# Kernel optimization log

Measured on AMD Instinct MI355X. Metric: run time of the kernel, lower is better.

Reference implementation:

```python
import jax, jax.numpy as jnp
import numpy as np

B, T, NG, NP, DV = 256, 100, 4096, 512, 2


def setup_inputs() -> dict:
    key = jax.random.key(0)
    k = jax.random.split(key, 6)
    v = jax.random.normal(k[0], (B, T, DV), dtype=jnp.float32) * 0.1
    P0 = jax.random.uniform(k[1], (B, NP), dtype=jnp.float32)
    # Dense kernels (glorot-ish scale); recurrent kernel uniform(-0.02, 0.02) per the module
    W_enc = jax.random.normal(k[2], (NP, NG), dtype=jnp.float32) / np.sqrt(NP)
    W_in = jax.random.normal(k[3], (DV, NG), dtype=jnp.float32) / np.sqrt(DV)
    W_rec = (jax.random.uniform(k[4], (NG, NG), dtype=jnp.float32) * 2.0 - 1.0) * 0.02
    W_dec = jax.random.normal(k[5], (NG, NP), dtype=jnp.float32) / np.sqrt(NG)
    return {"v": v, "P0": P0, "W_enc": W_enc, "W_in": W_in, "W_rec": W_rec, "W_dec": W_dec}


def reference(v, P0, W_enc, W_in, W_rec, W_dec):
    # encoder: init hidden state from place-cell code P0  -> [B, Ng]
    h0 = P0 @ W_enc
    # Precompute input projection for all timesteps: [B, T, Ng] -> scan over T
    xW = jnp.einsum('btd,dg->btg', v, W_in)
    xW_t = jnp.swapaxes(xW, 0, 1)  # [T, B, Ng]

    def step(h, x):
        h_new = jax.nn.relu(x + h @ W_rec)
        return h_new, h_new

    _, g = jax.lax.scan(step, h0, xW_t)      # g: [T, B, Ng]
    g = jnp.swapaxes(g, 0, 1)                # [B, T, Ng]
    place_preds = jnp.einsum('btg,gp->btp', g, W_dec)  # [B, T, Np]
    return place_preds
```

## Files before the change

### kernel.cpp

```cpp
#include <hip/hip_runtime.h>
#include <hip/hip_bf16.h>

typedef __attribute__((ext_vector_type(8))) short bf16x8;
typedef __attribute__((ext_vector_type(4))) float f32x4;

#define MFMA __builtin_amdgcn_mfma_f32_16x16x32_bf16

__device__ __forceinline__ short f2bf(float f) {
    union { __hip_bfloat16 h; short s; } u;
    u.h = __float2bfloat16(f);
    return u.s;
}

__device__ __forceinline__ void gld_lds16(const void* g, void* l) {
    auto gp = (const __attribute__((address_space(1))) void*)(g);
    auto lp = (__attribute__((address_space(3))) void*)(l);
    __builtin_amdgcn_global_load_lds(gp, lp, 16, 0, 0);
}

__global__ __launch_bounds__(64) void cvt_tile(const float* __restrict__ in,
                                               __hip_bfloat16* __restrict__ out, int C) {
    const int cd32 = C >> 5;
    const int tile = blockIdx.x;
    const int r16 = tile / cd32, c32 = tile - r16 * cd32;
    const int l = threadIdx.x;
    const int row = (r16 << 4) + (l & 15);
    const int c0 = (c32 << 5) + ((l >> 4) << 3);
    const float* src = in + (size_t)row * C + c0;
    short o[8];
#pragma unroll
    for (int j = 0; j < 8; ++j) o[j] = f2bf(src[j]);
    *(bf16x8*)((char*)out + (size_t)tile * 1024 + (l << 4)) = *(bf16x8*)o;
}

__global__ __launch_bounds__(64) void tcvt_tile(const float* __restrict__ in,
                                                __hip_bfloat16* __restrict__ out,
                                                int N, int K) {
    const int kd32 = K >> 5;
    const int tile = blockIdx.x;
    const int n16 = tile / kd32, k32 = tile - n16 * kd32;
    const int l = threadIdx.x;
    const int n = (n16 << 4) + (l & 15);
    const int k0 = (k32 << 5) + ((l >> 4) << 3);
    short o[8];
#pragma unroll
    for (int j = 0; j < 8; ++j) o[j] = f2bf(in[(size_t)(k0 + j) * N + n]);
    *(bf16x8*)((char*)out + (size_t)tile * 1024 + (l << 4)) = *(bf16x8*)o;
}

template <int MODE, int NW, int KC>
__global__ __launch_bounds__(NW * 64) void gemm_w(const __hip_bfloat16* __restrict__ A,
                                                  const __hip_bfloat16* __restrict__ B,
                                                  void* __restrict__ outp,
                                                  const float* __restrict__ v,
                                                  const float* __restrict__ Wi, int t) {
    constexpr int KD32 = KC * NW;
    __shared__ __align__(16) char lds[NW * 16384];
    const int id = blockIdx.x;
    int bm, bn;
    if constexpr (MODE == 2) {
        int xcd = id & 7, idx = id >> 3;
        int sw = xcd * 400 + idx;
        bm = sw >> 3;
        bn = sw & 7;
    } else {
        int xcd = id & 7, j = id >> 3;
        bn = (xcd << 3) + (j & 7);
        bm = j >> 3;
    }
    const int tid = threadIdx.x, wv = tid >> 6, lane = tid & 63;
    char* myl = lds + (wv << 14);
    const int kw0 = wv * KC;
    const int bm4 = bm << 2, bn4 = bn << 2;

    constexpr size_t FSTR = (size_t)KD32 << 10;
    const char* pA = (const char*)A + (((size_t)(bm4 * KD32 + kw0)) << 10) + (lane << 4);
    const char* pB = (const char*)B + (((size_t)(bn4 * KD32 + kw0)) << 10) + (lane << 4);

    f32x4 acc[4][4] = {};
    bf16x8 A00, A01, A02, A03, A10, A11, A12, A13,
           A20, A21, A22, A23, A30, A31, A32, A33;

#define STAGEB(SLOT, KI)                                   \
    do {                                                   \
        const char* pb_ = pB + ((size_t)(KI) << 10);       \
        char* d_ = myl + ((SLOT) << 12);                   \
        gld_lds16(pb_, d_);                                \
        gld_lds16(pb_ + FSTR, d_ + 1024);                  \
        gld_lds16(pb_ + 2 * FSTR, d_ + 2048);              \
        gld_lds16(pb_ + 3 * FSTR, d_ + 3072);              \
    } while (0)

#define LOADA(S, KI)                                       \
    do {                                                   \
        const char* pa_ = pA + ((size_t)(KI) << 10);       \
        A##S##0 = *(const bf16x8*)(pa_);                   \
        A##S##1 = *(const bf16x8*)(pa_ + FSTR);            \
        A##S##2 = *(const bf16x8*)(pa_ + 2 * FSTR);        \
        A##S##3 = *(const bf16x8*)(pa_ + 3 * FSTR);        \
    } while (0)

#define COMPUTE(S)                                                    \
    do {                                                              \
        const char* bb_ = myl + ((S) << 12) + (lane << 4);            \
        bf16x8 b0 = *(const bf16x8*)(bb_);                            \
        bf16x8 b1 = *(const bf16x8*)(bb_ + 1024);                     \
        bf16x8 b2 = *(const bf16x8*)(bb_ + 2048);                     \
        bf16x8 b3 = *(const bf16x8*)(bb_ + 3072);                     \
        acc[0][0] = MFMA(A##S##0, b0, acc[0][0], 0, 0, 0);            \
        acc[0][1] = MFMA(A##S##0, b1, acc[0][1], 0, 0, 0);            \
        acc[0][2] = MFMA(A##S##0, b2, acc[0][2], 0, 0, 0);            \
        acc[0][3] = MFMA(A##S##0, b3, acc[0][3], 0, 0, 0);            \
        acc[1][0] = MFMA(A##S##1, b0, acc[1][0], 0, 0, 0);            \
        acc[1][1] = MFMA(A##S##1, b1, acc[1][1], 0, 0, 0);            \
        acc[1][2] = MFMA(A##S##1, b2, acc[1][2], 0, 0, 0);            \
        acc[1][3] = MFMA(A##S##1, b3, acc[1][3], 0, 0, 0);            \
        acc[2][0] = MFMA(A##S##2, b0, acc[2][0], 0, 0, 0);            \
        acc[2][1] = MFMA(A##S##2, b1, acc[2][1], 0, 0, 0);            \
        acc[2][2] = MFMA(A##S##2, b2, acc[2][2], 0, 0, 0);            \
        acc[2][3] = MFMA(A##S##2, b3, acc[2][3], 0, 0, 0);            \
        acc[3][0] = MFMA(A##S##3, b0, acc[3][0], 0, 0, 0);            \
        acc[3][1] = MFMA(A##S##3, b1, acc[3][1], 0, 0, 0);            \
        acc[3][2] = MFMA(A##S##3, b2, acc[3][2], 0, 0, 0);            \
        acc[3][3] = MFMA(A##S##3, b3, acc[3][3], 0, 0, 0);            \
    } while (0)

#define ITER(S, SP, VM, DOISS, KI)                                 \
    do {                                                           \
        asm volatile("s_waitcnt vmcnt(%0)" ::"i"(VM) : "memory");  \
        __builtin_amdgcn_sched_barrier(0);                         \
        if (DOISS) {                                               \
            STAGEB(SP, (KI) + 3);                                  \
            LOADA(SP, (KI) + 3);                                   \
        }                                                          \
        __builtin_amdgcn_sched_barrier(0);                         \
        COMPUTE(S);                                                \
    } while (0)

    STAGEB(0, 0); LOADA(0, 0);
    __builtin_amdgcn_sched_barrier(0);
    STAGEB(1, 1); LOADA(1, 1);
    __builtin_amdgcn_sched_barrier(0);
    STAGEB(2, 2); LOADA(2, 2);
    __builtin_amdgcn_sched_barrier(0);

    int s = 0;
    for (; s + 4 < KC; s += 4) {
        ITER(0, 3, 16, true, s + 0);
        ITER(1, 0, 16, true, s + 1);
        ITER(2, 1, 16, true, s + 2);
        ITER(3, 2, 16, true, s + 3);
    }
    ITER(0, 3, 16, true,  s + 0);
    ITER(1, 0, 16, false, s + 1);
    ITER(2, 1, 8,  false, s + 2);
    ITER(3, 2, 0,  false, s + 3);

#undef ITER
#undef COMPUTE
#undef LOADA
#undef STAGEB

#pragma unroll
    for (int f = 0; f < 4; ++f)
#pragma unroll
        for (int g = 0; g < 4; ++g)
            *(f32x4*)(myl + (((f << 2) + g) << 10) + (lane << 4)) = acc[f][g];
    __syncthreads();

    constexpr int FPW = 16 / NW;
    f32x4 fin[FPW];
#pragma unroll
    for (int q = 0; q < FPW; ++q) {
        const int fid = wv * FPW + q;
        f32x4 ssum = {};
#pragma unroll
        for (int w = 0; w < NW; ++w)
            ssum += *(const f32x4*)(lds + (w << 14) + (fid << 10) + (lane << 4));
        fin[q] = ssum;
    }

    if constexpr (MODE == 0 || MODE == 1) {
        char* O = (char*)outp;
#pragma unroll
        for (int q = 0; q < FPW; ++q) {
            const int fid = wv * FPW + q;
            const int fr = fid >> 2, g = fid & 3;
            const int rbase = (bm << 6) + (fr << 4) + ((lane >> 4) << 2);
            const int c = (bn << 6) + (g << 4) + (lane & 15);
#pragma unroll
            for (int j = 0; j < 4; ++j) {
                int r = rbase + j;
                float val = fin[q][j];
                if constexpr (MODE == 1) {
                    float v0 = v[(size_t)(r * 100 + t) * 2 + 0];
                    float v1 = v[(size_t)(r * 100 + t) * 2 + 1];
                    val = fmaxf(val + v0 * Wi[c] + v1 * Wi[4096 + c], 0.0f);
                }
                size_t off = ((size_t)(r >> 4) * 128 + (c >> 5)) * 1024 +
                             ((size_t)((r & 15) + (((c >> 3) & 3) << 4)) << 4) +
                             ((c & 7) << 1);
                *(short*)(O + off) = f2bf(val);
            }
        }
    } else {
        float* O = (float*)outp;
#pragma unroll
        for (int q = 0; q < FPW; ++q) {
            const int fid = wv * FPW + q;
            const int fr = fid >> 2, g = fid & 3;
            const int rbase = (bm << 6) + (fr << 4) + ((lane >> 4) << 2);
            const int c = (bn << 6) + (g << 4) + (lane & 15);
#pragma unroll
            for (int j = 0; j < 4; ++j) {
                int r = rbase + j;
                int tt = r >> 8;
                int b = r & 255;
                O[((size_t)b * 100 + tt) * 512 + c] = fin[q][j];
            }
        }
    }
}

extern "C" void kernel_launch(void* const* d_in, const int* in_sizes, int n_in,
                              void* d_out, int out_size, void* d_ws, size_t ws_size,
                              hipStream_t stream) {
    const float* v     = (const float*)d_in[0];
    const float* P0    = (const float*)d_in[1];
    const float* W_enc = (const float*)d_in[2];
    const float* W_in  = (const float*)d_in[3];
    const float* W_rec = (const float*)d_in[4];
    const float* W_dec = (const float*)d_in[5];
    float* out = (float*)d_out;

    char* ws = (char*)d_ws;
    __hip_bfloat16* Wrt = (__hip_bfloat16*)(ws + 0);
    __hip_bfloat16* Wet = (__hip_bfloat16*)(ws + 33554432);
    __hip_bfloat16* Wdt = (__hip_bfloat16*)(ws + 37748736);
    __hip_bfloat16* P0t = (__hip_bfloat16*)(ws + 41943040);
    __hip_bfloat16* h0  = (__hip_bfloat16*)(ws + 42205184);
    __hip_bfloat16* G   = (__hip_bfloat16*)(ws + 44302336);

    tcvt_tile<<<32768, 64, 0, stream>>>(W_rec, Wrt, 4096, 4096);
    tcvt_tile<<<4096, 64, 0, stream>>>(W_enc, Wet, 4096, 512);
    tcvt_tile<<<4096, 64, 0, stream>>>(W_dec, Wdt, 512, 4096);
    cvt_tile<<<256, 64, 0, stream>>>(P0, P0t, 512);

    gemm_w<0, 4, 4><<<256, 256, 0, stream>>>(P0t, Wet, (void*)h0, nullptr, nullptr, 0);

    for (int t = 0; t < 100; ++t) {
        const __hip_bfloat16* hprev = (t == 0) ? h0 : (G + (size_t)(t - 1) * 1048576);
        gemm_w<1, 8, 16><<<256, 512, 0, stream>>>(hprev, Wrt,
                                                  (void*)(G + (size_t)t * 1048576), v, W_in, t);
    }

    gemm_w<2, 8, 16><<<3200, 512, 0, stream>>>(G, Wdt, (void*)out, nullptr, nullptr, 0);
}
```

Before: 1.666 ms.

## Load B operands directly to registers and use LDS-tiled transpose conversion

```diff
diff --git a/kernel.cpp b/kernel.cpp
--- a/kernel.cpp
+++ b/kernel.cpp
@@ -10,12 +10,6 @@
     union { __hip_bfloat16 h; short s; } u;
     u.h = __float2bfloat16(f);
     return u.s;
-}
-
-__device__ __forceinline__ void gld_lds16(const void* g, void* l) {
-    auto gp = (const __attribute__((address_space(1))) void*)(g);
-    auto lp = (__attribute__((address_space(3))) void*)(l);
-    __builtin_amdgcn_global_load_lds(gp, lp, 16, 0, 0);
 }
 
 __global__ __launch_bounds__(64) void cvt_tile(const float* __restrict__ in,
@@ -33,23 +27,41 @@
     *(bf16x8*)((char*)out + (size_t)tile * 1024 + (l << 4)) = *(bf16x8*)o;
 }
 
-__global__ __launch_bounds__(64) void tcvt_tile(const float* __restrict__ in,
-                                                __hip_bfloat16* __restrict__ out,
-                                                int N, int K) {
+__global__ __launch_bounds__(256) void tcvt256(const float* __restrict__ in,
+                                               __hip_bfloat16* __restrict__ out,
+                                               int N, int K) {
+    __shared__ float tile[64][65];
+    const int r0 = blockIdx.x << 6;
+    const int c0 = blockIdx.y << 6;
+    const int tid = threadIdx.x;
+    const int row = tid >> 2, cq = tid & 3;
+#pragma unroll
+    for (int it = 0; it < 4; ++it) {
+        int c4 = cq + (it << 2);
+        float4 vv = *(const float4*)(in + (size_t)(r0 + row) * N + c0 + (c4 << 2));
+        tile[row][(c4 << 2) + 0] = vv.x;
+        tile[row][(c4 << 2) + 1] = vv.y;
+        tile[row][(c4 << 2) + 2] = vv.z;
+        tile[row][(c4 << 2) + 3] = vv.w;
+    }
+    __syncthreads();
     const int kd32 = K >> 5;
-    const int tile = blockIdx.x;
-    const int n16 = tile / kd32, k32 = tile - n16 * kd32;
-    const int l = threadIdx.x;
-    const int n = (n16 << 4) + (l & 15);
-    const int k0 = (k32 << 5) + ((l >> 4) << 3);
-    short o[8];
-#pragma unroll
-    for (int j = 0; j < 8; ++j) o[j] = f2bf(in[(size_t)(k0 + j) * N + n]);
-    *(bf16x8*)((char*)out + (size_t)tile * 1024 + (l << 4)) = *(bf16x8*)o;
+#pragma unroll
+    for (int half = 0; half < 2; ++half) {
+        int slot = tid + (half << 8);
+        int ti = slot >> 6, l = slot & 63;
+        int ci = ti & 3, ri = ti >> 2;
+        short o[8];
+#pragma unroll
+        for (int j = 0; j < 8; ++j)
+            o[j] = f2bf(tile[(ri << 5) + ((l >> 4) << 3) + j][(ci << 4) + (l & 15)]);
+        size_t tidx = (size_t)((c0 >> 4) + ci) * kd32 + (r0 >> 5) + ri;
+        *(bf16x8*)((char*)out + tidx * 1024 + (l << 4)) = *(bf16x8*)o;
+    }
 }
 
 template <int MODE, int NW, int KC>
-__global__ __launch_bounds__(NW * 64) void gemm_w(const __hip_bfloat16* __restrict__ A,
+__global__ __launch_bounds__(NW * 64) void gemm_r(const __hip_bfloat16* __restrict__ A,
                                                   const __hip_bfloat16* __restrict__ B,
                                                   void* __restrict__ outp,
                                                   const float* __restrict__ v,
@@ -80,86 +92,73 @@
     f32x4 acc[4][4] = {};
     bf16x8 A00, A01, A02, A03, A10, A11, A12, A13,
            A20, A21, A22, A23, A30, A31, A32, A33;
-
-#define STAGEB(SLOT, KI)                                   \
-    do {                                                   \
-        const char* pb_ = pB + ((size_t)(KI) << 10);       \
-        char* d_ = myl + ((SLOT) << 12);                   \
-        gld_lds16(pb_, d_);                                \
-        gld_lds16(pb_ + FSTR, d_ + 1024);                  \
-        gld_lds16(pb_ + 2 * FSTR, d_ + 2048);              \
-        gld_lds16(pb_ + 3 * FSTR, d_ + 3072);              \
-    } while (0)
-
-#define LOADA(S, KI)                                       \
+    bf16x8 B00, B01, B02, B03, B10, B11, B12, B13,
+           B20, B21, B22, B23, B30, B31, B32, B33;
+
+#define LOADG(S, KI)                                       \
     do {                                                   \
         const char* pa_ = pA + ((size_t)(KI) << 10);       \
+        const char* pb_ = pB + ((size_t)(KI) << 10);       \
         A##S##0 = *(const bf16x8*)(pa_);                   \
         A##S##1 = *(const bf16x8*)(pa_ + FSTR);            \
         A##S##2 = *(const bf16x8*)(pa_ + 2 * FSTR);        \
         A##S##3 = *(const bf16x8*)(pa_ + 3 * FSTR);        \
+        B##S##0 = *(const bf16x8*)(pb_);                   \
+        B##S##1 = *(const bf16x8*)(pb_ + FSTR);            \
+        B##S##2 = *(const bf16x8*)(pb_ + 2 * FSTR);        \
+        B##S##3 = *(const bf16x8*)(pb_ + 3 * FSTR);        \
     } while (0)
 
-#define COMPUTE(S)                                                    \
-    do {                                                              \
-        const char* bb_ = myl + ((S) << 12) + (lane << 4);            \
-        bf16x8 b0 = *(const bf16x8*)(bb_);                            \
-        bf16x8 b1 = *(const bf16x8*)(bb_ + 1024);                     \
-        bf16x8 b2 = *(const bf16x8*)(bb_ + 2048);                     \
-        bf16x8 b3 = *(const bf16x8*)(bb_ + 3072);                     \
-        acc[0][0] = MFMA(A##S##0, b0, acc[0][0], 0, 0, 0);            \
-        acc[0][1] = MFMA(A##S##0, b1, acc[0][1], 0, 0, 0);            \
-        acc[0][2] = MFMA(A##S##0, b2, acc[0][2], 0, 0, 0);            \
-        acc[0][3] = MFMA(A##S##0, b3, acc[0][3], 0, 0, 0);            \
-        acc[1][0] = MFMA(A##S##1, b0, acc[1][0], 0, 0, 0);            \
-        acc[1][1] = MFMA(A##S##1, b1, acc[1][1], 0, 0, 0);            \
-        acc[1][2] = MFMA(A##S##1, b2, acc[1][2], 0, 0, 0);            \
-        acc[1][3] = MFMA(A##S##1, b3, acc[1][3], 0, 0, 0);            \
-        acc[2][0] = MFMA(A##S##2, b0, acc[2][0], 0, 0, 0);            \
-        acc[2][1] = MFMA(A##S##2, b1, acc[2][1], 0, 0, 0);            \
-        acc[2][2] = MFMA(A##S##2, b2, acc[2][2], 0, 0, 0);            \
-        acc[2][3] = MFMA(A##S##2, b3, acc[2][3], 0, 0, 0);            \
-        acc[3][0] = MFMA(A##S##3, b0, acc[3][0], 0, 0, 0);            \
-        acc[3][1] = MFMA(A##S##3, b1, acc[3][1], 0, 0, 0);            \
-        acc[3][2] = MFMA(A##S##3, b2, acc[3][2], 0, 0, 0);            \
-        acc[3][3] = MFMA(A##S##3, b3, acc[3][3], 0, 0, 0);            \
+#define COMPUTE(S)                                             \
+    do {                                                       \
+        acc[0][0] = MFMA(A##S##0, B##S##0, acc[0][0], 0, 0, 0);\
+        acc[0][1] = MFMA(A##S##0, B##S##1, acc[0][1], 0, 0, 0);\
+        acc[0][2] = MFMA(A##S##0, B##S##2, acc[0][2], 0, 0, 0);\
+        acc[0][3] = MFMA(A##S##0, B##S##3, acc[0][3], 0, 0, 0);\
+        acc[1][0] = MFMA(A##S##1, B##S##0, acc[1][0], 0, 0, 0);\
+        acc[1][1] = MFMA(A##S##1, B##S##1, acc[1][1], 0, 0, 0);\
+        acc[1][2] = MFMA(A##S##1, B##S##2, acc[1][2], 0, 0, 0);\
+        acc[1][3] = MFMA(A##S##1, B##S##3, acc[1][3], 0, 0, 0);\
+        acc[2][0] = MFMA(A##S##2, B##S##0, acc[2][0], 0, 0, 0);\
+        acc[2][1] = MFMA(A##S##2, B##S##1, acc[2][1], 0, 0, 0);\
+        acc[2][2] = MFMA(A##S##2, B##S##2, acc[2][2], 0, 0, 0);\
+        acc[2][3] = MFMA(A##S##2, B##S##3, acc[2][3], 0, 0, 0);\
+        acc[3][0] = MFMA(A##S##3, B##S##0, acc[3][0], 0, 0, 0);\
+        acc[3][1] = MFMA(A##S##3, B##S##1, acc[3][1], 0, 0, 0);\
+        acc[3][2] = MFMA(A##S##3, B##S##2, acc[3][2], 0, 0, 0);\
+        acc[3][3] = MFMA(A##S##3, B##S##3, acc[3][3], 0, 0, 0);\
     } while (0)
 
-#define ITER(S, SP, VM, DOISS, KI)                                 \
-    do {                                                           \
-        asm volatile("s_waitcnt vmcnt(%0)" ::"i"(VM) : "memory");  \
-        __builtin_amdgcn_sched_barrier(0);                         \
-        if (DOISS) {                                               \
-            STAGEB(SP, (KI) + 3);                                  \
-            LOADA(SP, (KI) + 3);                                   \
-        }                                                          \
-        __builtin_amdgcn_sched_barrier(0);                         \
-        COMPUTE(S);                                                \
+#define ITER(S, SP, DOISS, KI)                  \
+    do {                                        \
+        if (DOISS) LOADG(SP, (KI) + 3);         \
+        __builtin_amdgcn_sched_barrier(0);      \
+        COMPUTE(S);                             \
+        __builtin_amdgcn_sched_barrier(0);      \
     } while (0)
 
-    STAGEB(0, 0); LOADA(0, 0);
+    LOADG(0, 0);
     __builtin_amdgcn_sched_barrier(0);
-    STAGEB(1, 1); LOADA(1, 1);
+    LOADG(1, 1);
     __builtin_amdgcn_sched_barrier(0);
-    STAGEB(2, 2); LOADA(2, 2);
+    LOADG(2, 2);
     __builtin_amdgcn_sched_barrier(0);
 
     int s = 0;
     for (; s + 4 < KC; s += 4) {
-        ITER(0, 3, 16, true, s + 0);
-        ITER(1, 0, 16, true, s + 1);
-        ITER(2, 1, 16, true, s + 2);
-        ITER(3, 2, 16, true, s + 3);
-    }
-    ITER(0, 3, 16, true,  s + 0);
-    ITER(1, 0, 16, false, s + 1);
-    ITER(2, 1, 8,  false, s + 2);
-    ITER(3, 2, 0,  false, s + 3);
+        ITER(0, 3, true, s + 0);
+        ITER(1, 0, true, s + 1);
+        ITER(2, 1, true, s + 2);
+        ITER(3, 2, true, s + 3);
+    }
+    ITER(0, 3, true,  s + 0);
+    ITER(1, 0, false, s + 1);
+    ITER(2, 1, false, s + 2);
+    ITER(3, 2, false, s + 3);
 
 #undef ITER
 #undef COMPUTE
-#undef LOADA
-#undef STAGEB
+#undef LOADG
 
 #pragma unroll
     for (int f = 0; f < 4; ++f)
@@ -241,18 +240,18 @@
     __hip_bfloat16* h0  = (__hip_bfloat16*)(ws + 42205184);
     __hip_bfloat16* G   = (__hip_bfloat16*)(ws + 44302336);
 
-    tcvt_tile<<<32768, 64, 0, stream>>>(W_rec, Wrt, 4096, 4096);
-    tcvt_tile<<<4096, 64, 0, stream>>>(W_enc, Wet, 4096, 512);
-    tcvt_tile<<<4096, 64, 0, stream>>>(W_dec, Wdt, 512, 4096);
+    tcvt256<<<dim3(64, 64), 256, 0, stream>>>(W_rec, Wrt, 4096, 4096);
+    tcvt256<<<dim3(8, 64), 256, 0, stream>>>(W_enc, Wet, 4096, 512);
+    tcvt256<<<dim3(64, 8), 256, 0, stream>>>(W_dec, Wdt, 512, 4096);
     cvt_tile<<<256, 64, 0, stream>>>(P0, P0t, 512);
 
-    gemm_w<0, 4, 4><<<256, 256, 0, stream>>>(P0t, Wet, (void*)h0, nullptr, nullptr, 0);
+    gemm_r<0, 4, 4><<<256, 256, 0, stream>>>(P0t, Wet, (void*)h0, nullptr, nullptr, 0);
 
     for (int t = 0; t < 100; ++t) {
         const __hip_bfloat16* hprev = (t == 0) ? h0 : (G + (size_t)(t - 1) * 1048576);
-        gemm_w<1, 8, 16><<<256, 512, 0, stream>>>(hprev, Wrt,
+        gemm_r<1, 4, 32><<<256, 256, 0, stream>>>(hprev, Wrt,
                                                   (void*)(G + (size_t)t * 1048576), v, W_in, t);
     }
 
-    gemm_w<2, 8, 16><<<3200, 512, 0, stream>>>(G, Wdt, (void*)out, nullptr, nullptr, 0);
-}
+    gemm_r<2, 4, 32><<<3200, 256, 0, stream>>>(G, Wdt, (void*)out, nullptr, nullptr, 0);
+}
```

Result: faster. 1.511 ms (-9.3%).
